# Kernel tuning notes

Hardware: AMD Instinct MI355X
Metric: run time of the kernel (lower is better)

Reference implementation:

```python
import jax, jax.numpy as jnp
import numpy as np

B, H, W = 64, 16, 16
DIMS = [2048, 1024, 512, 256, 128, 1]


def _target_fc(x, w, b):
    # x: [B, in, H, W]; w: [B, out, in, 1, 1]; b: [B, out]
    # Equivalent to grouped 1x1 conv2d with groups=B (per-sample FC over channels).
    y = jnp.einsum('boi,bihw->bohw', w[:, :, :, 0, 0], x)
    return y + b[:, :, None, None]


def setup_inputs() -> dict:
    key = jax.random.key(0)
    ks = jax.random.split(key, 11)
    inp = {'x': jax.random.normal(ks[0], (B, DIMS[0], H, W), dtype=jnp.float32)}
    for i in range(5):
        din, dout = DIMS[i], DIMS[i + 1]
        scale = 1.0 / np.sqrt(din)
        inp[f'w{i+1}'] = jax.random.normal(ks[1 + 2 * i], (B, dout, din, 1, 1), dtype=jnp.float32) * scale
        inp[f'b{i+1}'] = jax.random.normal(ks[2 + 2 * i], (B, dout), dtype=jnp.float32) * scale
    return inp


def reference(x, w1, b1, w2, b2, w3, b3, w4, b4, w5, b5):
    q = jax.nn.sigmoid(_target_fc(x, w1, b1))
    q = jax.nn.sigmoid(_target_fc(q, w2, b2))
    q = jax.nn.sigmoid(_target_fc(q, w3, b3))
    q = jax.nn.sigmoid(_target_fc(q, w4, b4))
    q = _target_fc(q, w5, b5)
    return jnp.squeeze(q)  # [B, H, W]
```

## Files before the change

### kernel.cpp

```cpp
#include <hip/hip_runtime.h>
#include <hip/hip_bf16.h>
#include <cstdint>

#define DEVINL __device__ __forceinline__

typedef __attribute__((ext_vector_type(8))) short bf16x8;
typedef __attribute__((ext_vector_type(4))) float f32x4;

DEVINL unsigned short bfbits(float f) {
    union { __hip_bfloat16 h; unsigned short s; } v;
    v.h = __float2bfloat16(f);
    return v.s;
}
DEVINL unsigned pk2(float a, float b) {
    return (unsigned)bfbits(a) | ((unsigned)bfbits(b) << 16);
}
DEVINL float bf2f(unsigned short h) {
    union { unsigned u; float f; } v; v.u = ((unsigned)h) << 16;
    return v.f;
}

constexpr int BN = 256, BK = 32;
constexpr int NSP  = 256;
constexpr int SBUF = 256 * 32;

__global__ __launch_bounds__(256)
void xpose(const float* __restrict__ x, unsigned short* __restrict__ xT)
{
    __shared__ float sh[64][65];
    const int b   = blockIdx.y;
    const int kt  = blockIdx.x & 31;
    const int ntb = blockIdx.x >> 5;
    const int k0 = kt * 64, n0 = ntb * 64;

    const int r = threadIdx.x >> 4;
    const int c = (threadIdx.x & 15) * 4;

    const float* xb = x + ((size_t)b * 2048 + k0) * 256 + n0;
#pragma unroll
    for (int i = 0; i < 4; ++i) {
        float4 v = *(const float4*)(xb + (size_t)(r + 16 * i) * 256 + c);
        sh[r + 16 * i][c + 0] = v.x;
        sh[r + 16 * i][c + 1] = v.y;
        sh[r + 16 * i][c + 2] = v.z;
        sh[r + 16 * i][c + 3] = v.w;
    }
    __syncthreads();
#pragma unroll
    for (int i = 0; i < 4; ++i) {
        const int rr = r + 16 * i;
        uint2 o;
        o.x = pk2(sh[c + 0][rr], sh[c + 1][rr]);
        o.y = pk2(sh[c + 2][rr], sh[c + 3][rr]);
        *(uint2*)(xT + ((size_t)b * NSP + n0 + rr) * 2048 + k0 + c) = o;
    }
}

__global__ __launch_bounds__(1024, 1)
void fc_gemm256(const float* __restrict__ Wt, const float* __restrict__ bias,
                const unsigned short* __restrict__ X, unsigned short* __restrict__ Yt,
                int M, int K)
{
    constexpr int BM    = 256;
    constexpr int SABUF = BM * 32;

    const int b  = blockIdx.x;
    const int m0 = blockIdx.y * BM;

    __shared__ __align__(128) unsigned short pool[2 * SABUF + 2 * SBUF];
    unsigned short* sA = pool;
    unsigned short* sB = pool + 2 * SABUF;

    const int tid  = threadIdx.x;
    const int lane = tid & 63;
    const int wid  = tid >> 6;
    const int wm   = (wid >> 2) * 64;
    const int wn   = (wid & 3) * 64;
    const int fr   = lane & 15;
    const int fo   = (lane >> 4) * 8;

    const int am = tid >> 2, ac = (tid & 3) * 8;
    const float* Wb = Wt + (size_t)b * M * K + (size_t)m0 * K + (size_t)am * K + ac;

    const int grow = wid * 16 + (lane >> 2);
    const int gchk = ((lane & 3) ^ ((lane >> 3) & 3)) * 8;
    const unsigned short* Xb = X + (size_t)b * NSP * K;

    const int bslot = ((lane >> 4) ^ ((fr >> 1) & 3)) * 8;

    const int NT = K / BK;

    float4 aS0, aS1;

#define LOADA(k0) { aS0 = *(const float4*)(Wb + (k0)); \
                    aS1 = *(const float4*)(Wb + (k0) + 4); }
#define STOREA(p) { uint4 w_; \
        w_.x = pk2(aS0.x, aS0.y); w_.y = pk2(aS0.z, aS0.w); \
        w_.z = pk2(aS1.x, aS1.y); w_.w = pk2(aS1.z, aS1.w); \
        *(uint4*)&sA[(p) * SABUF + am * 32 + ac] = w_; }
#define GLOADB(k0, p) { \
        const unsigned short* src_ = Xb + (size_t)grow * K + (k0) + gchk; \
        const unsigned short* dst_ = sB + (p) * SBUF + (wid * 16) * 32; \
        __builtin_amdgcn_global_load_lds( \
            (const __attribute__((address_space(1))) void*)src_, \
            (__attribute__((address_space(3))) void*)dst_, 16, 0, 0); }

    f32x4 acc[4][4] = {};

    GLOADB(0, 0)
    LOADA(0)
    STOREA(0)
    __syncthreads();

#pragma unroll 1
    for (int t = 0; t < NT; ++t) {
        const int p = t & 1;
        if (t + 1 < NT) { LOADA((t + 1) * BK) GLOADB((t + 1) * BK, p ^ 1) }

        bf16x8 af[4], bfv[4];
#pragma unroll
        for (int i = 0; i < 4; ++i)
            af[i] = *(const bf16x8*)&sA[p * SABUF + (wm + i * 16 + fr) * 32 + fo];
#pragma unroll
        for (int i = 0; i < 4; ++i)
            bfv[i] = *(const bf16x8*)&sB[p * SBUF + (wn + i * 16 + fr) * 32 + bslot];

#pragma unroll
        for (int mi = 0; mi < 4; ++mi)
#pragma unroll
            for (int ni = 0; ni < 4; ++ni)
                acc[mi][ni] = __builtin_amdgcn_mfma_f32_16x16x32_bf16(af[mi], bfv[ni], acc[mi][ni], 0, 0, 0);

        if (t + 1 < NT) STOREA(p ^ 1)

        __syncthreads();
    }
#undef LOADA
#undef STOREA
#undef GLOADB

    const int hi4 = (lane >> 4) * 4;
#pragma unroll
    for (int mi = 0; mi < 4; ++mi) {
#pragma unroll
        for (int ni = 0; ni < 4; ++ni) {
            const int n  = wn + ni * 16 + fr;
            const int mb = m0 + wm + mi * 16 + hi4;
            f32x4 v = acc[mi][ni];
            float y[4];
#pragma unroll
            for (int q = 0; q < 4; ++q) {
                float yv = v[q] + bias[(size_t)b * M + mb + q];
                y[q] = 1.0f / (1.0f + __expf(-yv));
            }
            uint2 o;
            o.x = pk2(y[0], y[1]);
            o.y = pk2(y[2], y[3]);
            *(uint2*)&Yt[((size_t)b * NSP + n) * M + mb] = o;
        }
    }
}

__global__ __launch_bounds__(512, 2)
void fc_gemm128(const float* __restrict__ Wt, const float* __restrict__ bias,
                const unsigned short* __restrict__ X, unsigned short* __restrict__ Yt,
                int M, int K)
{
    constexpr int BM    = 128;
    constexpr int SABUF = BM * 32;

    const int b  = blockIdx.x;
    const int m0 = blockIdx.y * BM;

    __shared__ __align__(128) unsigned short pool[2 * SABUF + 2 * SBUF];
    unsigned short* sA = pool;
    unsigned short* sB = pool + 2 * SABUF;

    const int tid  = threadIdx.x;
    const int lane = tid & 63;
    const int wid  = tid >> 6;
    const int wm   = (wid >> 2) * 64;
    const int wn   = (wid & 3) * 64;
    const int fr   = lane & 15;
    const int fo   = (lane >> 4) * 8;

    const int am = tid >> 2, ac = (tid & 3) * 8;
    const float* Wb = Wt + (size_t)b * M * K + (size_t)m0 * K + (size_t)am * K + ac;

    const int grow = wid * 32 + (lane >> 2);
    const int gchk = ((lane & 3) ^ ((lane >> 3) & 3)) * 8;
    const unsigned short* Xb = X + (size_t)b * NSP * K;

    const int bslot = ((lane >> 4) ^ ((fr >> 1) & 3)) * 8;

    const int NT = K / BK;

    float4 aS0, aS1;

#define LOADA(k0) { aS0 = *(const float4*)(Wb + (k0)); \
                    aS1 = *(const float4*)(Wb + (k0) + 4); }
#define STOREA(p) { uint4 w_; \
        w_.x = pk2(aS0.x, aS0.y); w_.y = pk2(aS0.z, aS0.w); \
        w_.z = pk2(aS1.x, aS1.y); w_.w = pk2(aS1.z, aS1.w); \
        *(uint4*)&sA[(p) * SABUF + am * 32 + ac] = w_; }
#define GLOADB(k0, p) { \
    _Pragma("unroll") for (int i = 0; i < 2; ++i) { \
        const unsigned short* src_ = Xb + (size_t)(grow + i * 16) * K + (k0) + gchk; \
        const unsigned short* dst_ = sB + (p) * SBUF + (wid * 32 + i * 16) * 32; \
        __builtin_amdgcn_global_load_lds( \
            (const __attribute__((address_space(1))) void*)src_, \
            (__attribute__((address_space(3))) void*)dst_, 16, 0, 0); } }

    f32x4 acc[4][4] = {};

    GLOADB(0, 0)
    LOADA(0)
    STOREA(0)
    __syncthreads();

#pragma unroll 1
    for (int t = 0; t < NT; ++t) {
        const int p = t & 1;
        if (t + 1 < NT) { LOADA((t + 1) * BK) GLOADB((t + 1) * BK, p ^ 1) }

        bf16x8 af[4], bfv[4];
#pragma unroll
        for (int i = 0; i < 4; ++i)
            af[i] = *(const bf16x8*)&sA[p * SABUF + (wm + i * 16 + fr) * 32 + fo];
#pragma unroll
        for (int i = 0; i < 4; ++i)
            bfv[i] = *(const bf16x8*)&sB[p * SBUF + (wn + i * 16 + fr) * 32 + bslot];

#pragma unroll
        for (int mi = 0; mi < 4; ++mi)
#pragma unroll
            for (int ni = 0; ni < 4; ++ni)
                acc[mi][ni] = __builtin_amdgcn_mfma_f32_16x16x32_bf16(af[mi], bfv[ni], acc[mi][ni], 0, 0, 0);

        if (t + 1 < NT) STOREA(p ^ 1)

        __syncthreads();
    }
#undef LOADA
#undef STOREA
#undef GLOADB

    const int hi4 = (lane >> 4) * 4;
#pragma unroll
    for (int mi = 0; mi < 4; ++mi) {
#pragma unroll
        for (int ni = 0; ni < 4; ++ni) {
            const int n  = wn + ni * 16 + fr;
            const int mb = m0 + wm + mi * 16 + hi4;
            f32x4 v = acc[mi][ni];
            float y[4];
#pragma unroll
            for (int q = 0; q < 4; ++q) {
                float yv = v[q] + bias[(size_t)b * M + mb + q];
                y[q] = 1.0f / (1.0f + __expf(-yv));
            }
            uint2 o;
            o.x = pk2(y[0], y[1]);
            o.y = pk2(y[2], y[3]);
            *(uint2*)&Yt[((size_t)b * NSP + n) * M + mb] = o;
        }
    }
}

__global__ __launch_bounds__(256, 4)
void fc_gemm(const float* __restrict__ Wt, const float* __restrict__ bias,
             const unsigned short* __restrict__ X, unsigned short* __restrict__ Yt,
             int M, int K)
{
    constexpr int BM    = 64;
    constexpr int SABUF = BM * 32;

    const int b  = blockIdx.x;
    const int m0 = blockIdx.y * BM;

    __shared__ __align__(128) unsigned short pool[2 * SABUF + 2 * SBUF];
    unsigned short* sA = pool;
    unsigned short* sB = pool + 2 * SABUF;

    const int tid  = threadIdx.x;
    const int lane = tid & 63;
    const int wid  = tid >> 6;
    const int wn   = wid * 64;
    const int fr   = lane & 15;
    const int fo   = (lane >> 4) * 8;

    const int am = tid >> 2, ac = (tid & 3) * 8;
    const float* Wb = Wt + (size_t)b * M * K + (size_t)m0 * K + (size_t)am * K + ac;

    const int grow = wid * 64 + (lane >> 2);
    const int gchk = ((lane & 3) ^ ((lane >> 3) & 3)) * 8;
    const unsigned short* Xb = X + (size_t)b * NSP * K;

    const int bslot = ((lane >> 4) ^ ((fr >> 1) & 3)) * 8;

    const int NT = K / BK;

    float4 aS0, aS1;

#define LOADA(k0) { aS0 = *(const float4*)(Wb + (k0)); \
                    aS1 = *(const float4*)(Wb + (k0) + 4); }
#define STOREA(p) { uint4 w_; \
        w_.x = pk2(aS0.x, aS0.y); w_.y = pk2(aS0.z, aS0.w); \
        w_.z = pk2(aS1.x, aS1.y); w_.w = pk2(aS1.z, aS1.w); \
        *(uint4*)&sA[(p) * SABUF + am * 32 + ac] = w_; }
#define GLOADB(k0, p) { \
    _Pragma("unroll") for (int i = 0; i < 4; ++i) { \
        const unsigned short* src_ = Xb + (size_t)(grow + i * 16) * K + (k0) + gchk; \
        const unsigned short* dst_ = sB + (p) * SBUF + (wid * 64 + i * 16) * 32; \
        __builtin_amdgcn_global_load_lds( \
            (const __attribute__((address_space(1))) void*)src_, \
            (__attribute__((address_space(3))) void*)dst_, 16, 0, 0); } }

    f32x4 acc[4][4] = {};

    GLOADB(0, 0)
    LOADA(0)
    STOREA(0)
    __syncthreads();

#pragma unroll 1
    for (int t = 0; t < NT; ++t) {
        const int p = t & 1;
        if (t + 1 < NT) { LOADA((t + 1) * BK) GLOADB((t + 1) * BK, p ^ 1) }

        bf16x8 af[4], bfv[4];
#pragma unroll
        for (int i = 0; i < 4; ++i)
            af[i] = *(const bf16x8*)&sA[p * SABUF + (i * 16 + fr) * 32 + fo];
#pragma unroll
        for (int i = 0; i < 4; ++i)
            bfv[i] = *(const bf16x8*)&sB[p * SBUF + (wn + i * 16 + fr) * 32 + bslot];

#pragma unroll
        for (int mi = 0; mi < 4; ++mi)
#pragma unroll
            for (int ni = 0; ni < 4; ++ni)
                acc[mi][ni] = __builtin_amdgcn_mfma_f32_16x16x32_bf16(af[mi], bfv[ni], acc[mi][ni], 0, 0, 0);

        if (t + 1 < NT) STOREA(p ^ 1)

        __syncthreads();
    }
#undef LOADA
#undef STOREA
#undef GLOADB

    const int hi4 = (lane >> 4) * 4;
#pragma unroll
    for (int mi = 0; mi < 4; ++mi) {
#pragma unroll
        for (int ni = 0; ni < 4; ++ni) {
            const int n  = wn + ni * 16 + fr;
            const int mb = m0 + mi * 16 + hi4;
            f32x4 v = acc[mi][ni];
            float y[4];
#pragma unroll
            for (int q = 0; q < 4; ++q) {
                float yv = v[q] + bias[(size_t)b * M + mb + q];
                y[q] = 1.0f / (1.0f + __expf(-yv));
            }
            uint2 o;
            o.x = pk2(y[0], y[1]);
            o.y = pk2(y[2], y[3]);
            *(uint2*)&Yt[((size_t)b * NSP + n) * M + mb] = o;
        }
    }
}

__global__ void fc_final(const unsigned short* __restrict__ A4,
                         const float* __restrict__ W5,
                         const float* __restrict__ B5,
                         float* __restrict__ out)
{
    const int b = blockIdx.x;
    const int t = threadIdx.x;
    const unsigned short* row = A4 + ((size_t)b * NSP + t) * 128;
    const float* w = W5 + (size_t)b * 128;
    float acc = B5[b];
#pragma unroll
    for (int k = 0; k < 128; k += 8) {
        uint4 v = *(const uint4*)(row + k);
        acc += bf2f((unsigned short)(v.x & 0xffff)) * w[k+0];
        acc += bf2f((unsigned short)(v.x >> 16))    * w[k+1];
        acc += bf2f((unsigned short)(v.y & 0xffff)) * w[k+2];
        acc += bf2f((unsigned short)(v.y >> 16))    * w[k+3];
        acc += bf2f((unsigned short)(v.z & 0xffff)) * w[k+4];
        acc += bf2f((unsigned short)(v.z >> 16))    * w[k+5];
        acc += bf2f((unsigned short)(v.w & 0xffff)) * w[k+6];
        acc += bf2f((unsigned short)(v.w >> 16))    * w[k+7];
    }
    out[b * NSP + t] = acc;
}

extern "C" void kernel_launch(void* const* d_in, const int* in_sizes, int n_in,
                              void* d_out, int out_size, void* d_ws, size_t ws_size,
                              hipStream_t stream)
{
    const float* x  = (const float*)d_in[0];
    const float* w1 = (const float*)d_in[1];
    const float* b1 = (const float*)d_in[2];
    const float* w2 = (const float*)d_in[3];
    const float* b2 = (const float*)d_in[4];
    const float* w3 = (const float*)d_in[5];
    const float* b3 = (const float*)d_in[6];
    const float* w4 = (const float*)d_in[7];
    const float* b4 = (const float*)d_in[8];
    const float* w5 = (const float*)d_in[9];
    const float* b5 = (const float*)d_in[10];

    unsigned short* ws0 = (unsigned short*)d_ws;

    const size_t XT = (size_t)64 * 256 * 2048;
    unsigned short* xT   = ws0;
    unsigned short* act1 = ws0 + XT;
    unsigned short* act2 = ws0;
    unsigned short* act3 = ws0 + (size_t)64 * 256 * 512;
    unsigned short* act4 = ws0 + (size_t)64 * 256 * (512 + 256);

    xpose<<<dim3(128, 64), dim3(256), 0, stream>>>(x, xT);
    fc_gemm256<<<dim3(64, 4), dim3(1024), 0, stream>>>(w1, b1, xT,   act1, 1024, 2048);
    fc_gemm128<<<dim3(64, 4), dim3(512),  0, stream>>>(w2, b2, act1, act2,  512, 1024);
    fc_gemm<<<dim3(64, 4), dim3(256), 0, stream>>>(w3, b3, act2, act3,  256,  512);
    fc_gemm<<<dim3(64, 2), dim3(256), 0, stream>>>(w4, b4, act3, act4,  128,  256);
    fc_final<<<dim3(64), dim3(256), 0, stream>>>(act4, w5, b5, (float*)d_out);
}
```

Before: 302.0 us.

## Fuse layer-4 GEMM with final 128-to-1 projection in one kernel

Replaces the separate layer-4 grouped GEMM and the final dot-product kernel with one kernel per sample. That kernel computes the full 128x256 tile with MFMA, applies bias and sigmoid, stages the bf16 activations in shared memory, and reduces them against W5 with lane shuffles. This removes one launch and the global round trip of act4. In exchange, only 64 blocks run for layer 4 (previously 128), which lowers parallelism for that stage.

After: 305.6 us. About the same (+1.2%).

```diff
diff --git a/kernel.cpp b/kernel.cpp
--- a/kernel.cpp
+++ b/kernel.cpp
@@ -372,29 +372,143 @@
     }
 }
 
-__global__ void fc_final(const unsigned short* __restrict__ A4,
-                         const float* __restrict__ W5,
-                         const float* __restrict__ B5,
-                         float* __restrict__ out)
+__global__ __launch_bounds__(512, 2)
+void fc_gemm_l45(const float* __restrict__ Wt, const float* __restrict__ bias,
+                 const unsigned short* __restrict__ X,
+                 const float* __restrict__ W5, const float* __restrict__ B5,
+                 float* __restrict__ out)
 {
+    constexpr int BM    = 128;
+    constexpr int M     = 128;
+    constexpr int K     = 256;
+    constexpr int SABUF = BM * 32;
+    constexpr int EPP   = 136;
+
     const int b = blockIdx.x;
-    const int t = threadIdx.x;
-    const unsigned short* row = A4 + ((size_t)b * NSP + t) * 128;
-    const float* w = W5 + (size_t)b * 128;
-    float acc = B5[b];
-#pragma unroll
-    for (int k = 0; k < 128; k += 8) {
-        uint4 v = *(const uint4*)(row + k);
-        acc += bf2f((unsigned short)(v.x & 0xffff)) * w[k+0];
-        acc += bf2f((unsigned short)(v.x >> 16))    * w[k+1];
-        acc += bf2f((unsigned short)(v.y & 0xffff)) * w[k+2];
-        acc += bf2f((unsigned short)(v.y >> 16))    * w[k+3];
-        acc += bf2f((unsigned short)(v.z & 0xffff)) * w[k+4];
-        acc += bf2f((unsigned short)(v.z >> 16))    * w[k+5];
-        acc += bf2f((unsigned short)(v.w & 0xffff)) * w[k+6];
-        acc += bf2f((unsigned short)(v.w >> 16))    * w[k+7];
-    }
-    out[b * NSP + t] = acc;
+
+    __shared__ __align__(128) unsigned short pool[2 * SABUF + 2 * SBUF];
+    unsigned short* sA = pool;
+    unsigned short* sB = pool + 2 * SABUF;
+
+    const int tid  = threadIdx.x;
+    const int lane = tid & 63;
+    const int wid  = tid >> 6;
+    const int wm   = (wid >> 2) * 64;
+    const int wn   = (wid & 3) * 64;
+    const int fr   = lane & 15;
+    const int fo   = (lane >> 4) * 8;
+
+    const int am = tid >> 2, ac = (tid & 3) * 8;
+    const float* Wb = Wt + (size_t)b * M * K + (size_t)am * K + ac;
+
+    const int grow = wid * 32 + (lane >> 2);
+    const int gchk = ((lane & 3) ^ ((lane >> 3) & 3)) * 8;
+    const unsigned short* Xb = X + (size_t)b * NSP * K;
+
+    const int bslot = ((lane >> 4) ^ ((fr >> 1) & 3)) * 8;
+
+    const int NT = K / BK;
+
+    float4 aS0, aS1;
+
+#define LOADA(k0) { aS0 = *(const float4*)(Wb + (k0)); \
+                    aS1 = *(const float4*)(Wb + (k0) + 4); }
+#define STOREA(p) { uint4 w_; \
+        w_.x = pk2(aS0.x, aS0.y); w_.y = pk2(aS0.z, aS0.w); \
+        w_.z = pk2(aS1.x, aS1.y); w_.w = pk2(aS1.z, aS1.w); \
+        *(uint4*)&sA[(p) * SABUF + am * 32 + ac] = w_; }
+#define GLOADB(k0, p) { \
+    _Pragma("unroll") for (int i = 0; i < 2; ++i) { \
+        const unsigned short* src_ = Xb + (size_t)(grow + i * 16) * K + (k0) + gchk; \
+        const unsigned short* dst_ = sB + (p) * SBUF + (wid * 32 + i * 16) * 32; \
+        __builtin_amdgcn_global_load_lds( \
+            (const __attribute__((address_space(1))) void*)src_, \
+            (__attribute__((address_space(3))) void*)dst_, 16, 0, 0); } }
+
+    f32x4 acc[4][4] = {};
+
+    GLOADB(0, 0)
+    LOADA(0)
+    STOREA(0)
+    __syncthreads();
+
+#pragma unroll 1
+    for (int t = 0; t < NT; ++t) {
+        const int p = t & 1;
+        if (t + 1 < NT) { LOADA((t + 1) * BK) GLOADB((t + 1) * BK, p ^ 1) }
+
+        bf16x8 af[4], bfv[4];
+#pragma unroll
+        for (int i = 0; i < 4; ++i)
+            af[i] = *(const bf16x8*)&sA[p * SABUF + (wm + i * 16 + fr) * 32 + fo];
+#pragma unroll
+        for (int i = 0; i < 4; ++i)
+            bfv[i] = *(const bf16x8*)&sB[p * SBUF + (wn + i * 16 + fr) * 32 + bslot];
+
+#pragma unroll
+        for (int mi = 0; mi < 4; ++mi)
+#pragma unroll
+            for (int ni = 0; ni < 4; ++ni)
+                acc[mi][ni] = __builtin_amdgcn_mfma_f32_16x16x32_bf16(af[mi], bfv[ni], acc[mi][ni], 0, 0, 0);
+
+        if (t + 1 < NT) STOREA(p ^ 1)
+
+        __syncthreads();
+    }
+#undef LOADA
+#undef STOREA
+#undef GLOADB
+
+    const int hi4 = (lane >> 4) * 4;
+    const float* w5b = W5 + (size_t)b * 128;
+    const float  b5v = B5[b];
+#pragma unroll 1
+    for (int ph = 0; ph < 2; ++ph) {
+        __syncthreads();
+        if ((wn >> 7) == ph) {
+#pragma unroll
+            for (int mi = 0; mi < 4; ++mi) {
+#pragma unroll
+                for (int ni = 0; ni < 4; ++ni) {
+                    const int r  = (wn & 127) + ni * 16 + fr;
+                    const int mb = wm + mi * 16 + hi4;
+                    f32x4 v = acc[mi][ni];
+                    float y[4];
+#pragma unroll
+                    for (int q = 0; q < 4; ++q) {
+                        float yv = v[q] + bias[(size_t)b * M + mb + q];
+                        y[q] = 1.0f / (1.0f + __expf(-yv));
+                    }
+                    uint2 o;
+                    o.x = pk2(y[0], y[1]);
+                    o.y = pk2(y[2], y[3]);
+                    *(uint2*)&pool[r * EPP + mb] = o;
+                }
+            }
+        }
+        __syncthreads();
+        const int r = tid >> 2;
+        const int q = tid & 3;
+        const unsigned short* rowp = &pool[r * EPP + q * 32];
+        const float* wq = w5b + q * 32;
+        float s = 0.0f;
+#pragma unroll
+        for (int k = 0; k < 32; k += 8) {
+            uint4 v = *(const uint4*)(rowp + k);
+            s += bf2f((unsigned short)(v.x & 0xffff)) * wq[k + 0];
+            s += bf2f((unsigned short)(v.x >> 16))    * wq[k + 1];
+            s += bf2f((unsigned short)(v.y & 0xffff)) * wq[k + 2];
+            s += bf2f((unsigned short)(v.y >> 16))    * wq[k + 3];
+            s += bf2f((unsigned short)(v.z & 0xffff)) * wq[k + 4];
+            s += bf2f((unsigned short)(v.z >> 16))    * wq[k + 5];
+            s += bf2f((unsigned short)(v.w & 0xffff)) * wq[k + 6];
+            s += bf2f((unsigned short)(v.w >> 16))    * wq[k + 7];
+        }
+        s += __shfl_xor(s, 1);
+        s += __shfl_xor(s, 2);
+        if (q == 0)
+            out[(size_t)b * NSP + ph * 128 + r] = s + b5v;
+    }
 }
 
 extern "C" void kernel_launch(void* const* d_in, const int* in_sizes, int n_in,
@@ -420,12 +534,10 @@
     unsigned short* act1 = ws0 + XT;
     unsigned short* act2 = ws0;
     unsigned short* act3 = ws0 + (size_t)64 * 256 * 512;
-    unsigned short* act4 = ws0 + (size_t)64 * 256 * (512 + 256);
 
     xpose<<<dim3(128, 64), dim3(256), 0, stream>>>(x, xT);
     fc_gemm256<<<dim3(64, 4), dim3(1024), 0, stream>>>(w1, b1, xT,   act1, 1024, 2048);
     fc_gemm128<<<dim3(64, 4), dim3(512),  0, stream>>>(w2, b2, act1, act2,  512, 1024);
     fc_gemm<<<dim3(64, 4), dim3(256), 0, stream>>>(w3, b3, act2, act3,  256,  512);
-    fc_gemm<<<dim3(64, 2), dim3(256), 0, stream>>>(w4, b4, act3, act4,  128,  256);
-    fc_final<<<dim3(64), dim3(256), 0, stream>>>(act4, w5, b5, (float*)d_out);
-}
+    fc_gemm_l45<<<dim3(64), dim3(512), 0, stream>>>(w4, b4, act3, w5, b5, (float*)d_out);
+}
```
